# Kernel tuning notes

Measured on AMD Instinct MI355X. Metric: run time of the kernel, lower is better.

## Reference

```python
import jax, jax.numpy as jnp
import numpy as np

FIELDS = 32
EMBED = 64
PAIRS = FIELDS * (FIELDS - 1) // 2  # 496
BATCH = 2048


def setup_inputs() -> dict:
    key = jax.random.key(0)
    k1, k2 = jax.random.split(key)
    x = jax.random.normal(k1, (BATCH, FIELDS, EMBED), dtype=jnp.float32)
    kernel = jax.random.normal(k2, (EMBED, PAIRS, EMBED), dtype=jnp.float32) * 0.05
    return {"x": x, "kernel": kernel}


def reference(x, kernel):
    # Pair enumeration (i<j) matching the python double loop order.
    iu, ju = jnp.triu_indices(FIELDS, k=1)
    p = x[:, iu, :]  # (B, P, E)
    q = x[:, ju, :]  # (B, P, E)
    # Original: kp[b,f,pr] = sum_e p[b,pr,e]*kernel[f,pr,e];
    # result[b,pr] = sum_f kp[b,f,pr]*q[b,pr,f]
    # => bilinear form per pair, fused as a single einsum.
    result = jnp.einsum('bpe,fpe,bpf->bp', p, kernel, q)
    return result
```

## Files before the change

kernel.cpp:

```cpp
#include <hip/hip_runtime.h>
#include <hip/hip_bf16.h>


constexpr int BATCH  = 2048;
constexpr int FIELDS = 32;
constexpr int EMBED  = 64;
constexpr int PAIRS  = FIELDS * (FIELDS - 1) / 2;

typedef __attribute__((ext_vector_type(8))) short  short8;
typedef __attribute__((ext_vector_type(4))) float  f32x4;

constexpr size_t KPN     = (size_t)PAIRS * 2 * 4 * 64 * 8;
constexpr size_t KPH_OFF = 0;
constexpr size_t KPL_OFF = KPN * 2;
constexpr size_t WS_NEED = KPL_OFF + KPN * 2;

__device__ __forceinline__ unsigned short f32_to_bf16_rne(float f) {
    unsigned int u = __float_as_uint(f);
    u = u + 0x7fffu + ((u >> 16) & 1u);
    return (unsigned short)(u >> 16);
}
__device__ __forceinline__ float bf16_bits_to_f32(unsigned short h) {
    return __uint_as_float(((unsigned int)h) << 16);
}
__device__ __forceinline__ void split8(const float* v, short8& h8, short8& l8) {
    #pragma unroll
    for (int j = 0; j < 8; ++j) {
        const unsigned short hb = f32_to_bf16_rne(v[j]);
        h8[j] = (short)hb;
        l8[j] = (short)f32_to_bf16_rne(v[j] - bf16_bits_to_f32(hb));
    }
}

__global__ __launch_bounds__(256) void pack_k_kernel(
    const float* __restrict__ kern,
    unsigned short* __restrict__ kph,
    unsigned short* __restrict__ kpl)
{
    const int t    = (int)blockIdx.x * 256 + (int)threadIdx.x;
    const int lane = t & 63;
    const int nc   = (t >> 6) & 3;
    const int ks   = (t >> 8) & 1;
    const int pair = t >> 9;
    const int e    = nc * 16 + (lane & 15);
    const int f0   = ks * 32 + (lane >> 4) * 8;

    float v[8];
    #pragma unroll
    for (int jj = 0; jj < 8; ++jj)
        v[jj] = kern[((size_t)(f0 + jj) * PAIRS + pair) * EMBED + e];

    short8 h8, l8;
    split8(v, h8, l8);
    *(short8*)(kph + (size_t)t * 8) = h8;
    *(short8*)(kpl + (size_t)t * 8) = l8;
}

__global__ __launch_bounds__(256, 1) void opn_mfma_kernel(
    const float* __restrict__ x,
    const unsigned short* __restrict__ kph,
    const unsigned short* __restrict__ kpl,
    float* __restrict__ out)
{
    const int bid  = (int)blockIdx.x;
    const int p    = bid >> 3;
    const int mt   = bid & 7;
    const int wave = (int)threadIdx.x >> 6;
    const int lane = (int)threadIdx.x & 63;
    const int Mb   = mt * 256 + wave * 64;
    const int g    = lane >> 4;
    const int c    = lane & 15;

    int i = 0, rem = p;
    while (rem >= FIELDS - 1 - i) { rem -= FIELDS - 1 - i; ++i; }
    const int jf = i + 1 + rem;

    float4 xa[4][2][2];
    #pragma unroll
    for (int mr = 0; mr < 4; ++mr) {
        const int row = Mb + mr * 16 + c;
        const float* base = x + ((size_t)row * FIELDS + jf) * EMBED;
        #pragma unroll
        for (int ks = 0; ks < 2; ++ks) {
            xa[mr][ks][0] = *(const float4*)(base + ks * 32 + g * 8);
            xa[mr][ks][1] = *(const float4*)(base + ks * 32 + g * 8 + 4);
        }
    }
    short8 bh[2][4], bl[2][4];
    #pragma unroll
    for (int ks = 0; ks < 2; ++ks)
        #pragma unroll
        for (int nc = 0; nc < 4; ++nc) {
            const size_t kidx = (((size_t)(p * 2 + ks) * 4 + nc) * 64 + lane) * 8;
            bh[ks][nc] = *(const short8*)(kph + kidx);
            bl[ks][nc] = *(const short8*)(kpl + kidx);
        }

    short8 ah[4][2], al[4][2];
    #pragma unroll
    for (int mr = 0; mr < 4; ++mr)
        #pragma unroll
        for (int ks = 0; ks < 2; ++ks) {
            const float4 a0 = xa[mr][ks][0], a1 = xa[mr][ks][1];
            const float v[8] = {a0.x, a0.y, a0.z, a0.w, a1.x, a1.y, a1.z, a1.w};
            split8(v, ah[mr][ks], al[mr][ks]);
        }

    f32x4 acc[4][4];
    #pragma unroll
    for (int mr = 0; mr < 4; ++mr)
        #pragma unroll
        for (int nc = 0; nc < 4; ++nc)
            acc[mr][nc] = (f32x4){0.f, 0.f, 0.f, 0.f};

    #pragma unroll
    for (int ks = 0; ks < 2; ++ks)
        #pragma unroll
        for (int mr = 0; mr < 4; ++mr)
            #pragma unroll
            for (int nc = 0; nc < 4; ++nc) {
                acc[mr][nc] = __builtin_amdgcn_mfma_f32_16x16x32_bf16(ah[mr][ks], bh[ks][nc], acc[mr][nc], 0, 0, 0);
                acc[mr][nc] = __builtin_amdgcn_mfma_f32_16x16x32_bf16(ah[mr][ks], bl[ks][nc], acc[mr][nc], 0, 0, 0);
                acc[mr][nc] = __builtin_amdgcn_mfma_f32_16x16x32_bf16(al[mr][ks], bh[ks][nc], acc[mr][nc], 0, 0, 0);
            }

    float z[4][4];
    #pragma unroll
    for (int mr = 0; mr < 4; ++mr)
        #pragma unroll
        for (int t = 0; t < 4; ++t)
            z[mr][t] = 0.f;

    const size_t xi_base = (size_t)i * EMBED + c;
    #pragma unroll
    for (int mr = 0; mr < 4; ++mr)
        #pragma unroll
        for (int t = 0; t < 4; ++t) {
            const int row = Mb + mr * 16 + 4 * g + t;
            const float* xi = x + (size_t)row * (FIELDS * EMBED) + xi_base;
            #pragma unroll
            for (int nc = 0; nc < 4; ++nc)
                z[mr][t] = fmaf(acc[mr][nc][t], xi[nc * 16], z[mr][t]);
        }

    #pragma unroll
    for (int mask = 1; mask < 16; mask <<= 1)
        #pragma unroll
        for (int mr = 0; mr < 4; ++mr)
            #pragma unroll
            for (int t = 0; t < 4; ++t)
                z[mr][t] += __shfl_xor(z[mr][t], mask, 64);

    if (c < 4) {
        const int t = c;
        #pragma unroll
        for (int mr = 0; mr < 4; ++mr) {
            const int row = Mb + mr * 16 + 4 * g + t;
            out[(size_t)row * PAIRS + p] = z[mr][t];
        }
    }
}

constexpr int BT     = 64;
constexpr int BTILES = BATCH / BT;

__global__ __launch_bounds__(64) void opn_fp32_kernel(
    const float* __restrict__ x,
    const float* __restrict__ kern,
    float* __restrict__ out)
{
    const int bid   = (int)blockIdx.x;
    const int p     = bid >> 5;
    const int btile = bid & (BTILES - 1);
    const int lane  = (int)threadIdx.x;
    const int b     = btile * BT + lane;

    int i = 0, rem = p;
    while (rem >= FIELDS - 1 - i) { rem -= FIELDS - 1 - i; ++i; }
    const int j = i + 1 + rem;

    const float* xrow_i = x + (size_t)b * (FIELDS * EMBED) + i * EMBED;
    const float* xrow_j = x + (size_t)b * (FIELDS * EMBED) + j * EMBED;
    const float* kp     = kern + (size_t)p * EMBED;

    float acc[EMBED];
    #pragma unroll
    for (int e = 0; e < EMBED; ++e) acc[e] = 0.0f;

    const float4* xj4 = (const float4*)xrow_j;
    #pragma unroll 2
    for (int f4 = 0; f4 < EMBED / 4; ++f4) {
        const float4 v = xj4[f4];
        const float xjf[4] = {v.x, v.y, v.z, v.w};
        #pragma unroll
        for (int s = 0; s < 4; ++s) {
            const float* kf = kp + (size_t)(f4 * 4 + s) * (PAIRS * EMBED);
            #pragma unroll
            for (int e = 0; e < EMBED; ++e)
                acc[e] = fmaf(xjf[s], kf[e], acc[e]);
        }
    }

    float r = 0.0f;
    const float4* xi4 = (const float4*)xrow_i;
    #pragma unroll
    for (int e4 = 0; e4 < EMBED / 4; ++e4) {
        const float4 u = xi4[e4];
        r = fmaf(u.x, acc[e4 * 4 + 0], r);
        r = fmaf(u.y, acc[e4 * 4 + 1], r);
        r = fmaf(u.z, acc[e4 * 4 + 2], r);
        r = fmaf(u.w, acc[e4 * 4 + 3], r);
    }
    out[(size_t)b * PAIRS + p] = r;
}

extern "C" void kernel_launch(void* const* d_in, const int* in_sizes, int n_in,
                              void* d_out, int out_size, void* d_ws, size_t ws_size,
                              hipStream_t stream) {
    const float* x    = (const float*)d_in[0];
    const float* kern = (const float*)d_in[1];
    float*       out  = (float*)d_out;

    if (ws_size < WS_NEED) {
        opn_fp32_kernel<<<dim3(PAIRS * BTILES), dim3(64), 0, stream>>>(x, kern, out);
        return;
    }

    char* ws = (char*)d_ws;
    unsigned short* kph = (unsigned short*)(ws + KPH_OFF);
    unsigned short* kpl = (unsigned short*)(ws + KPL_OFF);

    pack_k_kernel<<<dim3(PAIRS * 512 / 256), dim3(256), 0, stream>>>(kern, kph, kpl);
    opn_mfma_kernel<<<dim3(PAIRS * 8), dim3(256), 0, stream>>>(x, kph, kpl, out);
}
```

Baseline: 125.3 us.

## Fuse kernel packing into MFMA kernel via shared-memory bf16 split

Removes the separate pack kernel and workspace. Each block now loads its pair's kernel slice straight from global memory, splits it into hi/lo bf16 and stages it in shared memory before the MFMA loop. The hi part becomes a plain truncation instead of a round-to-nearest. Block ordering changes so blocks sharing a batch tile differ in pair, and the launch-bounds occupancy hint is relaxed. The cost is that each of the 8 batch-tile blocks per pair redoes the strided kernel load and split, plus an LDS round-trip and a barrier.

```diff
diff --git a/kernel.cpp b/kernel.cpp
--- a/kernel.cpp
+++ b/kernel.cpp
@@ -1,5 +1,4 @@
 #include <hip/hip_runtime.h>
-#include <hip/hip_bf16.h>
 
 
 constexpr int BATCH  = 2048;
@@ -10,70 +9,47 @@
 typedef __attribute__((ext_vector_type(8))) short  short8;
 typedef __attribute__((ext_vector_type(4))) float  f32x4;
 
-constexpr size_t KPN     = (size_t)PAIRS * 2 * 4 * 64 * 8;
-constexpr size_t KPH_OFF = 0;
-constexpr size_t KPL_OFF = KPN * 2;
-constexpr size_t WS_NEED = KPL_OFF + KPN * 2;
-
-__device__ __forceinline__ unsigned short f32_to_bf16_rne(float f) {
+__device__ __forceinline__ unsigned short bf16_rne(float f) {
     unsigned int u = __float_as_uint(f);
     u = u + 0x7fffu + ((u >> 16) & 1u);
     return (unsigned short)(u >> 16);
 }
-__device__ __forceinline__ float bf16_bits_to_f32(unsigned short h) {
-    return __uint_as_float(((unsigned int)h) << 16);
-}
-__device__ __forceinline__ void split8(const float* v, short8& h8, short8& l8) {
-    #pragma unroll
-    for (int j = 0; j < 8; ++j) {
-        const unsigned short hb = f32_to_bf16_rne(v[j]);
-        h8[j] = (short)hb;
-        l8[j] = (short)f32_to_bf16_rne(v[j] - bf16_bits_to_f32(hb));
-    }
-}
 
-__global__ __launch_bounds__(256) void pack_k_kernel(
+__global__ __launch_bounds__(256) void opn_fused_kernel(
+    const float* __restrict__ x,
     const float* __restrict__ kern,
-    unsigned short* __restrict__ kph,
-    unsigned short* __restrict__ kpl)
-{
-    const int t    = (int)blockIdx.x * 256 + (int)threadIdx.x;
-    const int lane = t & 63;
-    const int nc   = (t >> 6) & 3;
-    const int ks   = (t >> 8) & 1;
-    const int pair = t >> 9;
-    const int e    = nc * 16 + (lane & 15);
-    const int f0   = ks * 32 + (lane >> 4) * 8;
-
-    float v[8];
-    #pragma unroll
-    for (int jj = 0; jj < 8; ++jj)
-        v[jj] = kern[((size_t)(f0 + jj) * PAIRS + pair) * EMBED + e];
-
-    short8 h8, l8;
-    split8(v, h8, l8);
-    *(short8*)(kph + (size_t)t * 8) = h8;
-    *(short8*)(kpl + (size_t)t * 8) = l8;
-}
-
-__global__ __launch_bounds__(256, 1) void opn_mfma_kernel(
-    const float* __restrict__ x,
-    const unsigned short* __restrict__ kph,
-    const unsigned short* __restrict__ kpl,
     float* __restrict__ out)
 {
+    __shared__ unsigned short smem[8192];
+
+    const int tid  = (int)threadIdx.x;
+    const int lane = tid & 63;
+    const int wave = tid >> 6;
     const int bid  = (int)blockIdx.x;
-    const int p    = bid >> 3;
-    const int mt   = bid & 7;
-    const int wave = (int)threadIdx.x >> 6;
-    const int lane = (int)threadIdx.x & 63;
-    const int Mb   = mt * 256 + wave * 64;
+    const int p    = bid % PAIRS;
+    const int mt   = bid / PAIRS;
     const int g    = lane >> 4;
     const int c    = lane & 15;
+    const int Mb   = mt * 256 + wave * 64;
 
     int i = 0, rem = p;
     while (rem >= FIELDS - 1 - i) { rem -= FIELDS - 1 - i; ++i; }
     const int jf = i + 1 + rem;
+
+    float kv[2][8];
+    #pragma unroll
+    for (int h = 0; h < 2; ++h) {
+        const int idx = tid + h * 256;
+        const int ks = idx >> 8;
+        const int nc = (idx >> 6) & 3;
+        const int ln = idx & 63;
+        const int f0 = ks * 32 + (ln >> 4) * 8;
+        const int e  = nc * 16 + (ln & 15);
+        const float* kbase = kern + (size_t)p * EMBED + e;
+        #pragma unroll
+        for (int jj = 0; jj < 8; ++jj)
+            kv[h][jj] = kbase[(size_t)(f0 + jj) * (PAIRS * EMBED)];
+    }
 
     float4 xa[4][2][2];
     #pragma unroll
@@ -86,15 +62,22 @@
             xa[mr][ks][1] = *(const float4*)(base + ks * 32 + g * 8 + 4);
         }
     }
-    short8 bh[2][4], bl[2][4];
+
     #pragma unroll
-    for (int ks = 0; ks < 2; ++ks)
+    for (int h = 0; h < 2; ++h) {
+        const int idx = tid + h * 256;
+        short8 h8, l8;
         #pragma unroll
-        for (int nc = 0; nc < 4; ++nc) {
-            const size_t kidx = (((size_t)(p * 2 + ks) * 4 + nc) * 64 + lane) * 8;
-            bh[ks][nc] = *(const short8*)(kph + kidx);
-            bl[ks][nc] = *(const short8*)(kpl + kidx);
+        for (int jj = 0; jj < 8; ++jj) {
+            const float v = kv[h][jj];
+            const unsigned int u = __float_as_uint(v);
+            h8[jj] = (short)(u >> 16);
+            l8[jj] = (short)bf16_rne(v - __uint_as_float(u & 0xffff0000u));
         }
+        *(short8*)(smem + idx * 8)        = h8;
+        *(short8*)(smem + 4096 + idx * 8) = l8;
+    }
+    __syncthreads();
 
     short8 ah[4][2], al[4][2];
     #pragma unroll
@@ -103,7 +86,12 @@
         for (int ks = 0; ks < 2; ++ks) {
             const float4 a0 = xa[mr][ks][0], a1 = xa[mr][ks][1];
             const float v[8] = {a0.x, a0.y, a0.z, a0.w, a1.x, a1.y, a1.z, a1.w};
-            split8(v, ah[mr][ks], al[mr][ks]);
+            #pragma unroll
+            for (int jj = 0; jj < 8; ++jj) {
+                const unsigned int u = __float_as_uint(v[jj]);
+                ah[mr][ks][jj] = (short)(u >> 16);
+                al[mr][ks][jj] = (short)bf16_rne(v[jj] - __uint_as_float(u & 0xffff0000u));
+            }
         }
 
     f32x4 acc[4][4];
@@ -114,15 +102,23 @@
             acc[mr][nc] = (f32x4){0.f, 0.f, 0.f, 0.f};
 
     #pragma unroll
-    for (int ks = 0; ks < 2; ++ks)
+    for (int ks = 0; ks < 2; ++ks) {
+        short8 bh[4], bl[4];
+        #pragma unroll
+        for (int nc = 0; nc < 4; ++nc) {
+            const int off = ((ks * 4 + nc) * 64 + lane) * 8;
+            bh[nc] = *(const short8*)(smem + off);
+            bl[nc] = *(const short8*)(smem + 4096 + off);
+        }
         #pragma unroll
         for (int mr = 0; mr < 4; ++mr)
             #pragma unroll
             for (int nc = 0; nc < 4; ++nc) {
-                acc[mr][nc] = __builtin_amdgcn_mfma_f32_16x16x32_bf16(ah[mr][ks], bh[ks][nc], acc[mr][nc], 0, 0, 0);
-                acc[mr][nc] = __builtin_amdgcn_mfma_f32_16x16x32_bf16(ah[mr][ks], bl[ks][nc], acc[mr][nc], 0, 0, 0);
-                acc[mr][nc] = __builtin_amdgcn_mfma_f32_16x16x32_bf16(al[mr][ks], bh[ks][nc], acc[mr][nc], 0, 0, 0);
+                acc[mr][nc] = __builtin_amdgcn_mfma_f32_16x16x32_bf16(ah[mr][ks], bh[nc], acc[mr][nc], 0, 0, 0);
+                acc[mr][nc] = __builtin_amdgcn_mfma_f32_16x16x32_bf16(ah[mr][ks], bl[nc], acc[mr][nc], 0, 0, 0);
+                acc[mr][nc] = __builtin_amdgcn_mfma_f32_16x16x32_bf16(al[mr][ks], bh[nc], acc[mr][nc], 0, 0, 0);
             }
+    }
 
     float z[4][4];
     #pragma unroll
@@ -161,59 +157,6 @@
     }
 }
 
-constexpr int BT     = 64;
-constexpr int BTILES = BATCH / BT;
-
-__global__ __launch_bounds__(64) void opn_fp32_kernel(
-    const float* __restrict__ x,
-    const float* __restrict__ kern,
-    float* __restrict__ out)
-{
-    const int bid   = (int)blockIdx.x;
-    const int p     = bid >> 5;
-    const int btile = bid & (BTILES - 1);
-    const int lane  = (int)threadIdx.x;
-    const int b     = btile * BT + lane;
-
-    int i = 0, rem = p;
-    while (rem >= FIELDS - 1 - i) { rem -= FIELDS - 1 - i; ++i; }
-    const int j = i + 1 + rem;
-
-    const float* xrow_i = x + (size_t)b * (FIELDS * EMBED) + i * EMBED;
-    const float* xrow_j = x + (size_t)b * (FIELDS * EMBED) + j * EMBED;
-    const float* kp     = kern + (size_t)p * EMBED;
-
-    float acc[EMBED];
-    #pragma unroll
-    for (int e = 0; e < EMBED; ++e) acc[e] = 0.0f;
-
-    const float4* xj4 = (const float4*)xrow_j;
-    #pragma unroll 2
-    for (int f4 = 0; f4 < EMBED / 4; ++f4) {
-        const float4 v = xj4[f4];
-        const float xjf[4] = {v.x, v.y, v.z, v.w};
-        #pragma unroll
-        for (int s = 0; s < 4; ++s) {
-            const float* kf = kp + (size_t)(f4 * 4 + s) * (PAIRS * EMBED);
-            #pragma unroll
-            for (int e = 0; e < EMBED; ++e)
-                acc[e] = fmaf(xjf[s], kf[e], acc[e]);
-        }
-    }
-
-    float r = 0.0f;
-    const float4* xi4 = (const float4*)xrow_i;
-    #pragma unroll
-    for (int e4 = 0; e4 < EMBED / 4; ++e4) {
-        const float4 u = xi4[e4];
-        r = fmaf(u.x, acc[e4 * 4 + 0], r);
-        r = fmaf(u.y, acc[e4 * 4 + 1], r);
-        r = fmaf(u.z, acc[e4 * 4 + 2], r);
-        r = fmaf(u.w, acc[e4 * 4 + 3], r);
-    }
-    out[(size_t)b * PAIRS + p] = r;
-}
-
 extern "C" void kernel_launch(void* const* d_in, const int* in_sizes, int n_in,
                               void* d_out, int out_size, void* d_ws, size_t ws_size,
                               hipStream_t stream) {
@@ -221,15 +164,5 @@
     const float* kern = (const float*)d_in[1];
     float*       out  = (float*)d_out;
 
-    if (ws_size < WS_NEED) {
-        opn_fp32_kernel<<<dim3(PAIRS * BTILES), dim3(64), 0, stream>>>(x, kern, out);
-        return;
-    }
-
-    char* ws = (char*)d_ws;
-    unsigned short* kph = (unsigned short*)(ws + KPH_OFF);
-    unsigned short* kpl = (unsigned short*)(ws + KPL_OFF);
-
-    pack_k_kernel<<<dim3(PAIRS * 512 / 256), dim3(256), 0, stream>>>(kern, kph, kpl);
-    opn_mfma_kernel<<<dim3(PAIRS * 8), dim3(256), 0, stream>>>(x, kph, kpl, out);
+    opn_fused_kernel<<<dim3(PAIRS * 8), dim3(256), 0, stream>>>(x, kern, out);
 }
```

New measurement: 126.4 us. Within noise of the previous version (+0.9%).
